# Optimization experiments

Hardware: AMD Instinct MI355X
Metric: run time of the kernel (lower is better)

The kernel has to match this reference:

```python
import jax, jax.numpy as jnp
import numpy as np

DIM = 2048
HEADS = 16
KV_HEADS = 4
DIM_HEAD = 128
INNER = HEADS * DIM_HEAD          # 2048
KV_INNER = KV_HEADS * DIM_HEAD    # 512
FF = 4 * DIM                      # 8192
QK_SCALE = 10.0                   # x-transformers default qk_norm_scale
B, S = 2, 2048


def layer_norm(x, g, b, eps=1e-5):
    m = jnp.mean(x, axis=-1, keepdims=True)
    v = jnp.mean((x - m) ** 2, axis=-1, keepdims=True)
    return (x - m) * jax.lax.rsqrt(v + eps) * g + b


def l2norm(t, eps=1e-12):
    n = jnp.sqrt(jnp.sum(t * t, axis=-1, keepdims=True))
    return t / jnp.maximum(n, eps)


def setup_inputs() -> dict:
    key = jax.random.key(0)
    ks = jax.random.split(key, 12)
    s = lambda fan_in: 1.0 / np.sqrt(fan_in)
    return {
        "x":     jax.random.normal(ks[0], (B, S, DIM), jnp.float32),
        "wq":    jax.random.normal(ks[1], (DIM, INNER), jnp.float32) * s(DIM),
        "wk":    jax.random.normal(ks[2], (DIM, KV_INNER), jnp.float32) * s(DIM),
        "wv":    jax.random.normal(ks[3], (DIM, KV_INNER), jnp.float32) * s(DIM),
        "wo":    jax.random.normal(ks[4], (INNER, DIM), jnp.float32) * s(INNER),
        "ln1_g": jnp.ones((DIM,), jnp.float32),
        "ln1_b": jnp.zeros((DIM,), jnp.float32),
        "w1":    jax.random.normal(ks[5], (DIM, FF), jnp.float32) * s(DIM),
        "b1":    jnp.zeros((FF,), jnp.float32),
        "lnf_g": jnp.ones((FF,), jnp.float32),
        "lnf_b": jnp.zeros((FF,), jnp.float32),
        "w2":    jax.random.normal(ks[6], (FF, DIM), jnp.float32) * s(FF),
        "b2":    jnp.zeros((DIM,), jnp.float32),
    }


def reference(x, wq, wk, wv, wo, ln1_g, ln1_b, w1, b1, lnf_g, lnf_b, w2, b2):
    b, s, _ = x.shape
    rep = HEADS // KV_HEADS
    # GQA projections
    q = (x @ wq).reshape(b, s, HEADS, DIM_HEAD).transpose(0, 2, 1, 3)      # [b,h,s,d]
    k = (x @ wk).reshape(b, s, KV_HEADS, DIM_HEAD).transpose(0, 2, 1, 3)   # [b,g,s,d]
    v = (x @ wv).reshape(b, s, KV_HEADS, DIM_HEAD).transpose(0, 2, 1, 3)
    # qk-norm: l2-normalize q/k along head dim, fixed scale
    q = l2norm(q)
    k = l2norm(k)
    k = jnp.repeat(k, rep, axis=1)  # expand kv heads to query heads
    v = jnp.repeat(v, rep, axis=1)
    scores = jnp.einsum("bhid,bhjd->bhij", q, k) * QK_SCALE
    attn = jax.nn.softmax(scores, axis=-1)
    o = jnp.einsum("bhij,bhjd->bhid", attn, v)
    o = o.transpose(0, 2, 1, 3).reshape(b, s, INNER) @ wo
    # post-attention LayerNorm (no residual in the source)
    h = layer_norm(o, ln1_g, ln1_b)
    # FFN: SiLU + post-activation LayerNorm (dropout inert in eval)
    f = jax.nn.silu(h @ w1 + b1)
    f = layer_norm(f, lnf_g, lnf_b)
    y = f @ w2 + b2
    # the source re-applies the SAME norm after the ffn
    return layer_norm(y, ln1_g, ln1_b)
```

## Files before the change

kernel.cpp:

```cpp
#include <hip/hip_runtime.h>


typedef __attribute__((ext_vector_type(8))) short short8;
typedef __attribute__((ext_vector_type(4))) float f32x4;
typedef __attribute__((ext_vector_type(16))) float f32x16;

__device__ __forceinline__ unsigned short f2bf(float f) {
  unsigned int u = __builtin_bit_cast(unsigned int, f);
  u += 0x7FFFu + ((u >> 16) & 1u);
  return (unsigned short)(u >> 16);
}
__device__ __forceinline__ float bf2f(unsigned short h) {
  unsigned int u = ((unsigned int)h) << 16;
  return __builtin_bit_cast(float, u);
}

typedef const void __attribute__((address_space(1)))* gas1_t;
typedef void __attribute__((address_space(3)))* las3_t;
#define GLDS16(g, l) \
  __builtin_amdgcn_global_load_lds((gas1_t)(const void*)(g), (las3_t)(void*)(l), 16, 0, 0)

__global__ __launch_bounds__(256) void cast_f32_bf16(const float* __restrict__ src,
                                                     unsigned short* __restrict__ dst,
                                                     int n) {
  int i = (blockIdx.x * 256 + threadIdx.x) * 4;
  if (i >= n) return;
  float4 f = *(const float4*)(src + i);
  uint2 u;
  u.x = (unsigned)f2bf(f.x) | ((unsigned)f2bf(f.y) << 16);
  u.y = (unsigned)f2bf(f.z) | ((unsigned)f2bf(f.w) << 16);
  *(uint2*)(dst + i) = u;
}

__global__ void transcast(const float* __restrict__ src, unsigned short* __restrict__ dst,
                          int R, int C, int dst_ld, int row_off) {
  __shared__ float t[32][33];
  const int tx = threadIdx.x, ty = threadIdx.y;
  const int c0 = blockIdx.x * 32, r0 = blockIdx.y * 32;
#pragma unroll
  for (int j = 0; j < 4; ++j)
    t[ty + j * 8][tx] = src[(size_t)(r0 + ty + j * 8) * C + c0 + tx];
  __syncthreads();
#pragma unroll
  for (int j = 0; j < 4; ++j)
    dst[(size_t)(row_off + c0 + ty + j * 8) * dst_ld + r0 + tx] = f2bf(t[tx][ty + j * 8]);
}

template <int KS>
__global__ __launch_bounds__(512, 1) void gemm8ph(const unsigned short* __restrict__ A,
                                                  const unsigned short* __restrict__ Bt,
                                                  unsigned short* __restrict__ C0,
                                                  unsigned short* __restrict__ C1,
                                                  int ldc, int Keff) {
  extern __shared__ char lds[];
  const int tid = threadIdx.x, l = tid & 63, w = tid >> 6;
  const int wr = w >> 2, wc = w & 3;
  const int gx = gridDim.x, gy = gridDim.y;
  const int did = blockIdx.y * gx + blockIdx.x;
  const int q = (gx * gy) >> 3;
  const int tcm = (did & 7) * q + (did >> 3);
  const int brow = (tcm % gy) * 256, bcol = (tcm / gy) * 256;
  const int ld = Keff * KS;
  const unsigned short* Aa = A + (size_t)brow * ld + blockIdx.z * Keff;
  const unsigned short* Bb = Bt + (size_t)bcol * ld + blockIdx.z * Keff;
  unsigned short* C = (KS == 1 || blockIdx.z == 0) ? C0 : C1;
  const int NT = Keff >> 6;

  const int slot = l >> 4;
  const int rowA = wr * 128 + (l & 15);
  const int aRd = ((((rowA << 2) | slot) << 4) ^ ((rowA & 7) << 4));
  const int rowB = wc * 64 + (l & 15);
  const int bRd = ((((rowB << 2) | slot) << 4) ^ ((rowB & 7) << 4));

  f32x4 acc[8][4];
#pragma unroll
  for (int m = 0; m < 8; ++m)
#pragma unroll
    for (int n = 0; n < 4; ++n) acc[m][n] = (f32x4){0.f, 0.f, 0.f, 0.f};

  auto stage = [&](int s) {
    const int tile = s >> 2, kind = s & 3;
    const int kofs = ((tile < NT) ? tile * 64 : 0) + (kind >> 1) * 32;
    const unsigned short* src = (kind & 1) ? Bb : Aa;
    char* dst = lds + (tile & 1) * 65536 + kind * 16384;
#pragma unroll
    for (int r = 0; r < 2; ++r) {
      const int g = r * 512 + tid;
      const int rw = ((g >> 3) << 1) | (((g >> 2) ^ (g >> 4)) & 1);
      const int sl = (g ^ rw) & 3;
      GLDS16(src + (size_t)rw * ld + kofs + sl * 8, dst + g * 16);
    }
  };

  stage(0); stage(1); stage(2); stage(3); stage(4); stage(5);
  asm volatile("s_waitcnt vmcnt(4)" ::: "memory");
  __builtin_amdgcn_s_barrier();

  for (int T = 0; T < NT; ++T) {
    char* cur = lds + (T & 1) * 65536;
#pragma unroll
    for (int ph = 0; ph < 4; ++ph) {
      const int ks = ph >> 1, mh = ph & 1;
      char* abase = cur + ks * 32768;
      char* bbase = cur + 16384 + ks * 32768;
      short8 af[4], bf[4];
#pragma unroll
      for (int n = 0; n < 4; ++n) bf[n] = *(const short8*)(bbase + bRd + n * 1024);
#pragma unroll
      for (int m = 0; m < 4; ++m) af[m] = *(const short8*)(abase + aRd + (mh * 4 + m) * 1024);
      stage(4 * T + ph + 6);
      __builtin_amdgcn_s_barrier();
      asm volatile("s_waitcnt lgkmcnt(0)" ::: "memory");
      __builtin_amdgcn_sched_barrier(0);
      __builtin_amdgcn_s_setprio(1);
#pragma unroll
      for (int m = 0; m < 4; ++m)
#pragma unroll
        for (int n = 0; n < 4; ++n)
          acc[mh * 4 + m][n] =
              __builtin_amdgcn_mfma_f32_16x16x32_bf16(af[m], bf[n], acc[mh * 4 + m][n], 0, 0, 0);
      __builtin_amdgcn_s_setprio(0);
      if (ph == 3) asm volatile("s_waitcnt vmcnt(4)" ::: "memory");
      __builtin_amdgcn_s_barrier();
    }
  }

#pragma unroll
  for (int m = 0; m < 8; ++m)
#pragma unroll
    for (int r = 0; r < 4; ++r) {
      const int row = brow + wr * 128 + m * 16 + (l >> 4) * 4 + r;
#pragma unroll
      for (int n = 0; n < 4; ++n) {
        const int col = bcol + wc * 64 + n * 16 + (l & 15);
        C[(size_t)row * ldc + col] = f2bf(acc[m][n][r]);
      }
    }
}

__global__ __launch_bounds__(256) void l2norm_qk(unsigned short* __restrict__ qkv) {
  const int wid = blockIdx.x * 4 + (threadIdx.x >> 6);
  const int l = threadIdx.x & 63;
  const int token = wid / 20, u = wid % 20;
  const int col = (u < 16) ? u * 128 : 2048 + (u - 16) * 128;
  unsigned short* p = qkv + (size_t)token * 3072 + col + l * 2;
  const float a = bf2f(p[0]), b = bf2f(p[1]);
  float ss = a * a + b * b;
#pragma unroll
  for (int m = 1; m < 64; m <<= 1) ss += __shfl_xor(ss, m);
  const float sc = ((u < 16) ? 10.f : 1.f) / fmaxf(sqrtf(ss), 1e-12f);
  p[0] = f2bf(a * sc);
  p[1] = f2bf(b * sc);
}

__global__ __launch_bounds__(256) void vtrans(const unsigned short* __restrict__ qkv,
                                              unsigned short* __restrict__ vt) {
  const int idx = blockIdx.x * 256 + threadIdx.x;
  const int s_ = idx & 2047;
  const int rest = idx >> 11;
  const int d = rest & 127;
  const int bg = rest >> 7;
  const int b = bg >> 2, g = bg & 3;
  vt[idx] = qkv[(size_t)(b * 2048 + s_) * 3072 + 2560 + g * 128 + d];
}

__global__ __launch_bounds__(512) void attn_kernel(const unsigned short* __restrict__ qkv,
                                                   const unsigned short* __restrict__ vt,
                                                   unsigned short* __restrict__ out) {
  extern __shared__ char smem[];
  const int tid = threadIdx.x, w = tid >> 6, l = tid & 63;
  const int hi = l >> 5, l31 = l & 31;

  const int n = blockIdx.x;
  const int np = (n & 7) * 32 + (n >> 3);
  const int qi = np & 7, bh = np >> 3;
  const int b = bh >> 4, h = bh & 15, g = h >> 2;
  const int q0 = qi * 256;

  const unsigned short* kbase = qkv + (size_t)(b * 2048) * 3072 + 2048 + g * 128;
  const unsigned short* vbase = vt + (size_t)(b * 4 + g) * 128 * 2048;

  short8 qf[8];
  {
    const unsigned short* qrow = qkv + (size_t)(b * 2048 + q0 + w * 32 + l31) * 3072 + h * 128;
#pragma unroll
    for (int st = 0; st < 8; ++st)
      qf[st] = *(const short8*)&qrow[st * 16 + hi * 8];
  }

  f32x16 o[4];
#pragma unroll
  for (int d0 = 0; d0 < 4; ++d0)
#pragma unroll
    for (int i = 0; i < 16; ++i) o[d0][i] = 0.f;
  float l_part = 0.f;

  const int krow = tid >> 3, kc = (tid & 7) * 2;
  const int vd = tid >> 2, vc = (tid & 3) * 2;
  const unsigned short* kg = kbase + (size_t)krow * 3072 + kc * 8;
  const unsigned short* vg = vbase + (size_t)vd * 2048 + vc * 8;
  const int ko0 = krow * 256 + ((kc ^ (krow & 15)) << 4);
  const int ko1 = krow * 256 + (((kc + 1) ^ (krow & 15)) << 4);
  const int vrp = vd >> 1, vcl = (vd & 1) * 8;
  const int vo0 = vrp * 256 + (((vcl + vc) ^ (vrp & 15)) << 4);
  const int vo1 = vrp * 256 + (((vcl + vc + 1) ^ (vrp & 15)) << 4);

  {
    uint4 k0 = *(const uint4*)kg, k1 = *(const uint4*)(kg + 8);
    uint4 v0 = *(const uint4*)vg, v1 = *(const uint4*)(vg + 8);
    char* Kb = smem;
    char* Vb = smem + 16384;
    *(uint4*)(Kb + ko0) = k0; *(uint4*)(Kb + ko1) = k1;
    *(uint4*)(Vb + vo0) = v0; *(uint4*)(Vb + vo1) = v1;
  }
  __syncthreads();

  const int swzk = l31 & 15;
  for (int t = 0; t < 32; ++t) {
    uint4 k0, k1, v0, v1;
    const bool more = (t + 1) < 32;
    if (more) {
      const size_t kvo = (size_t)(t + 1) * 64;
      k0 = *(const uint4*)(kg + kvo * 3072);
      k1 = *(const uint4*)(kg + kvo * 3072 + 8);
      v0 = *(const uint4*)(vg + kvo);
      v1 = *(const uint4*)(vg + kvo + 8);
    }

    char* Kb = smem + (t & 1) * 32768;
    char* Vb = Kb + 16384;

    f32x16 s0, s1;
#pragma unroll
    for (int i = 0; i < 16; ++i) { s0[i] = 0.f; s1[i] = 0.f; }
    __builtin_amdgcn_s_setprio(1);
#pragma unroll
    for (int st = 0; st < 8; ++st) {
      const int ch = st * 2 + hi;
      short8 kf0 = *(const short8*)(Kb + l31 * 256 + ((ch ^ swzk) << 4));
      short8 kf1 = *(const short8*)(Kb + (l31 + 32) * 256 + ((ch ^ swzk) << 4));
      s0 = __builtin_amdgcn_mfma_f32_32x32x16_bf16(kf0, qf[st], s0, 0, 0, 0);
      s1 = __builtin_amdgcn_mfma_f32_32x32x16_bf16(kf1, qf[st], s1, 0, 0, 0);
    }
    __builtin_amdgcn_s_setprio(0);

#pragma unroll
    for (int i = 0; i < 16; ++i) {
      s0[i] = __expf(s0[i] - 10.f);
      s1[i] = __expf(s1[i] - 10.f);
      l_part += s0[i] + s1[i];
    }

    short8 pa[4];
#pragma unroll
    for (int ks = 0; ks < 4; ++ks) {
      const f32x16& sv = (ks < 2) ? s0 : s1;
      const int base = (ks & 1) * 8;
      auto pk = [](float x, float y) -> unsigned {
        unsigned ux = __builtin_bit_cast(unsigned, x);
        unsigned uy = __builtin_bit_cast(unsigned, y);
        return ((uy + 0x8000u) & 0xFFFF0000u) | ((ux + 0x8000u) >> 16);
      };
      unsigned a = pk(sv[base + 0], sv[base + 1]);
      unsigned bq = pk(sv[base + 4], sv[base + 5]);
      unsigned c = pk(sv[base + 2], sv[base + 3]);
      unsigned d = pk(sv[base + 6], sv[base + 7]);
      unsigned as = __shfl_xor(a, 32), bs = __shfl_xor(bq, 32);
      unsigned cs = __shfl_xor(c, 32), ds = __shfl_xor(d, 32);
      uint4 wv;
      wv.x = (l < 32) ? a : bs;
      wv.y = (l < 32) ? c : ds;
      wv.z = (l < 32) ? as : bq;
      wv.w = (l < 32) ? cs : d;
      pa[ks] = __builtin_bit_cast(short8, wv);
    }

    __builtin_amdgcn_s_setprio(1);
#pragma unroll
    for (int ks = 0; ks < 4; ++ks) {
#pragma unroll
      for (int d0 = 0; d0 < 4; ++d0) {
        const int dd = d0 * 32 + l31;
        const int rp = dd >> 1;
        const int cl = ((dd & 1) * 8 + ks * 2 + hi) ^ (rp & 15);
        short8 vf = *(const short8*)(Vb + rp * 256 + (cl << 4));
        o[d0] = __builtin_amdgcn_mfma_f32_32x32x16_bf16(pa[ks], vf, o[d0], 0, 0, 0);
      }
    }
    __builtin_amdgcn_s_setprio(0);

    __syncthreads();
    if (more) {
      char* Kn = smem + ((t + 1) & 1) * 32768;
      char* Vn = Kn + 16384;
      *(uint4*)(Kn + ko0) = k0; *(uint4*)(Kn + ko1) = k1;
      *(uint4*)(Vn + vo0) = v0; *(uint4*)(Vn + vo1) = v1;
    }
    __syncthreads();
  }

  float ltot = l_part + __shfl_xor(l_part, 32);
  float linv = 1.f / ltot;
  const int tok_base = b * 2048 + q0 + w * 32;
#pragma unroll
  for (int r = 0; r < 16; ++r) {
    const int qr = (r & 3) + 8 * (r >> 2) + 4 * hi;
    const float li = __shfl(linv, qr);
    unsigned short* orow = out + (size_t)(tok_base + qr) * 2048 + h * 128 + l31;
#pragma unroll
    for (int d0 = 0; d0 < 4; ++d0)
      orow[d0 * 32] = f2bf(o[d0][r] * li);
  }
}

template <int NC, bool BIAS, bool SILU, bool OUTF32, bool SUM2>
__global__ __launch_bounds__(256) void ln_row(const unsigned short* __restrict__ src,
                                              const unsigned short* __restrict__ src2,
                                              unsigned short* __restrict__ dstb,
                                              float* __restrict__ dstf,
                                              const float* __restrict__ gamma,
                                              const float* __restrict__ beta,
                                              const float* __restrict__ bias) {
  constexpr int E = NC / 256;
  const int row = blockIdx.x, tid = threadIdx.x;
  const size_t base = (size_t)row * NC + tid * E;
  float v[E];
#pragma unroll
  for (int c = 0; c < E / 8; ++c) {
    uint4 u = *(const uint4*)(src + base + c * 8);
    const unsigned short* us = (const unsigned short*)&u;
#pragma unroll
    for (int j = 0; j < 8; ++j) v[c * 8 + j] = bf2f(us[j]);
  }
  if constexpr (SUM2) {
#pragma unroll
    for (int c = 0; c < E / 8; ++c) {
      uint4 u = *(const uint4*)(src2 + base + c * 8);
      const unsigned short* us = (const unsigned short*)&u;
#pragma unroll
      for (int j = 0; j < 8; ++j) v[c * 8 + j] += bf2f(us[j]);
    }
  }
  if constexpr (BIAS) {
#pragma unroll
    for (int i = 0; i < E; ++i) v[i] += bias[tid * E + i];
  }
  if constexpr (SILU) {
#pragma unroll
    for (int i = 0; i < E; ++i) v[i] = v[i] / (1.f + __expf(-v[i]));
  }
  float s = 0.f, q = 0.f;
#pragma unroll
  for (int i = 0; i < E; ++i) {
    s += v[i];
    q += v[i] * v[i];
  }
#pragma unroll
  for (int m = 1; m < 64; m <<= 1) {
    s += __shfl_xor(s, m);
    q += __shfl_xor(q, m);
  }
  __shared__ float rs[4], rq[4];
  if ((tid & 63) == 0) {
    rs[tid >> 6] = s;
    rq[tid >> 6] = q;
  }
  __syncthreads();
  s = rs[0] + rs[1] + rs[2] + rs[3];
  q = rq[0] + rq[1] + rq[2] + rq[3];
  const float mean = s / NC;
  const float rstd = rsqrtf(q / NC - mean * mean + 1e-5f);
#pragma unroll
  for (int i = 0; i < E; ++i)
    v[i] = (v[i] - mean) * rstd * gamma[tid * E + i] + beta[tid * E + i];
  if constexpr (OUTF32) {
#pragma unroll
    for (int c = 0; c < E / 4; ++c) {
      float4 f = {v[c * 4], v[c * 4 + 1], v[c * 4 + 2], v[c * 4 + 3]};
      *(float4*)(dstf + base + c * 4) = f;
    }
  } else {
#pragma unroll
    for (int c = 0; c < E / 8; ++c) {
      uint4 u;
      unsigned* up = (unsigned*)&u;
#pragma unroll
      for (int j = 0; j < 4; ++j)
        up[j] = (unsigned)f2bf(v[c * 8 + j * 2]) | ((unsigned)f2bf(v[c * 8 + j * 2 + 1]) << 16);
      *(uint4*)(dstb + base + c * 8) = u;
    }
  }
}

extern "C" void kernel_launch(void* const* d_in, const int* in_sizes, int n_in,
                              void* d_out, int out_size, void* d_ws, size_t ws_size,
                              hipStream_t stream) {
  (void)in_sizes; (void)n_in; (void)out_size; (void)ws_size;
  const float* x     = (const float*)d_in[0];
  const float* wq    = (const float*)d_in[1];
  const float* wk    = (const float*)d_in[2];
  const float* wv    = (const float*)d_in[3];
  const float* wo    = (const float*)d_in[4];
  const float* ln1_g = (const float*)d_in[5];
  const float* ln1_b = (const float*)d_in[6];
  const float* w1    = (const float*)d_in[7];
  const float* b1    = (const float*)d_in[8];
  const float* lnf_g = (const float*)d_in[9];
  const float* lnf_b = (const float*)d_in[10];
  const float* w2    = (const float*)d_in[11];
  const float* b2    = (const float*)d_in[12];

  unsigned short* ws = (unsigned short*)d_ws;
  unsigned short* wqkvT  = ws;
  unsigned short* woT    = wqkvT  + (size_t)3072 * 2048;
  unsigned short* w1T    = woT    + (size_t)2048 * 2048;
  unsigned short* w2T    = w1T    + (size_t)8192 * 2048;
  unsigned short* xb     = w2T    + (size_t)2048 * 8192;
  unsigned short* qkv    = xb     + (size_t)4096 * 2048;
  unsigned short* vt     = qkv    + (size_t)4096 * 3072;
  unsigned short* attn_o = vt     + (size_t)4096 * 512;
  unsigned short* f1     = attn_o + (size_t)4096 * 2048;

  (void)hipFuncSetAttribute((const void*)gemm8ph<1>,
                            hipFuncAttributeMaxDynamicSharedMemorySize, 131072);
  (void)hipFuncSetAttribute((const void*)gemm8ph<2>,
                            hipFuncAttributeMaxDynamicSharedMemorySize, 131072);
  (void)hipFuncSetAttribute((const void*)attn_kernel,
                            hipFuncAttributeMaxDynamicSharedMemorySize, 65536);

  const dim3 tb(32, 8);
  cast_f32_bf16<<<8192, 256, 0, stream>>>(x, xb, 4096 * 2048);
  transcast<<<dim3(64, 64),  tb, 0, stream>>>(wq, wqkvT, 2048, 2048, 2048, 0);
  transcast<<<dim3(16, 64),  tb, 0, stream>>>(wk, wqkvT, 2048, 512, 2048, 2048);
  transcast<<<dim3(16, 64),  tb, 0, stream>>>(wv, wqkvT, 2048, 512, 2048, 2560);
  transcast<<<dim3(64, 64),  tb, 0, stream>>>(wo, woT, 2048, 2048, 2048, 0);
  transcast<<<dim3(256, 64), tb, 0, stream>>>(w1, w1T, 2048, 8192, 2048, 0);
  transcast<<<dim3(64, 256), tb, 0, stream>>>(w2, w2T, 8192, 2048, 8192, 0);

  gemm8ph<1><<<dim3(12, 16, 1), 512, 131072, stream>>>(xb, wqkvT, qkv, nullptr, 3072, 2048);
  l2norm_qk<<<20480, 256, 0, stream>>>(qkv);
  vtrans<<<8192, 256, 0, stream>>>(qkv, vt);
  attn_kernel<<<256, 512, 65536, stream>>>(qkv, vt, attn_o);
  gemm8ph<2><<<dim3(8, 16, 2), 512, 131072, stream>>>(attn_o, woT, qkv, f1, 2048, 1024);
  ln_row<2048, false, false, false, true><<<4096, 256, 0, stream>>>(
      qkv, f1, xb, nullptr, ln1_g, ln1_b, nullptr);
  gemm8ph<1><<<dim3(32, 16, 1), 512, 131072, stream>>>(xb, w1T, f1, nullptr, 8192, 2048);
  ln_row<8192, true, true, false, false><<<4096, 256, 0, stream>>>(
      f1, nullptr, f1, nullptr, lnf_g, lnf_b, b1);
  gemm8ph<2><<<dim3(8, 16, 2), 512, 131072, stream>>>(f1, w2T, xb, attn_o, 2048, 4096);
  ln_row<2048, true, false, true, true><<<4096, 256, 0, stream>>>(
      xb, attn_o, nullptr, (float*)d_out, ln1_g, ln1_b, b2);
}
```

Measured before the change: 672.0 us.

## Software-pipeline LDS fragment reads ahead of MFMA phases in GEMM loop

Restructures the GEMM main loop so the LDS fragment loads for the next phase are issued before the current phase's 16 MFMAs. B fragments are also reused across the two M halves instead of being reloaded. The aim is to hide LDS read latency behind matrix math rather than stalling on lgkmcnt(0) before every MFMA batch. The cost is more live fragment registers, which may raise VGPR pressure, plus an extra barrier per phase.

```diff
diff --git a/kernel.cpp b/kernel.cpp
--- a/kernel.cpp
+++ b/kernel.cpp
@@ -92,38 +92,74 @@
     }
   };
 
+#define BAR() __builtin_amdgcn_s_barrier()
+#define LGKM0() do { asm volatile("s_waitcnt lgkmcnt(0)" ::: "memory"); \
+                     __builtin_amdgcn_sched_barrier(0); } while (0)
+#define SBAR() __builtin_amdgcn_sched_barrier(0)
+#define MFMA16(AF, BF, MO)                                                     \
+  do {                                                                         \
+    __builtin_amdgcn_s_setprio(1);                                             \
+    _Pragma("unroll") for (int m_ = 0; m_ < 4; ++m_)                           \
+        _Pragma("unroll") for (int n_ = 0; n_ < 4; ++n_)                       \
+            acc[(MO) + m_][n_] = __builtin_amdgcn_mfma_f32_16x16x32_bf16(      \
+                (AF)[m_], (BF)[n_], acc[(MO) + m_][n_], 0, 0, 0);              \
+    __builtin_amdgcn_s_setprio(0);                                             \
+  } while (0)
+
   stage(0); stage(1); stage(2); stage(3); stage(4); stage(5);
   asm volatile("s_waitcnt vmcnt(4)" ::: "memory");
-  __builtin_amdgcn_s_barrier();
+  BAR();
 
   for (int T = 0; T < NT; ++T) {
     char* cur = lds + (T & 1) * 65536;
-#pragma unroll
-    for (int ph = 0; ph < 4; ++ph) {
-      const int ks = ph >> 1, mh = ph & 1;
-      char* abase = cur + ks * 32768;
-      char* bbase = cur + 16384 + ks * 32768;
-      short8 af[4], bf[4];
-#pragma unroll
-      for (int n = 0; n < 4; ++n) bf[n] = *(const short8*)(bbase + bRd + n * 1024);
-#pragma unroll
-      for (int m = 0; m < 4; ++m) af[m] = *(const short8*)(abase + aRd + (mh * 4 + m) * 1024);
-      stage(4 * T + ph + 6);
-      __builtin_amdgcn_s_barrier();
-      asm volatile("s_waitcnt lgkmcnt(0)" ::: "memory");
-      __builtin_amdgcn_sched_barrier(0);
-      __builtin_amdgcn_s_setprio(1);
-#pragma unroll
-      for (int m = 0; m < 4; ++m)
-#pragma unroll
-        for (int n = 0; n < 4; ++n)
-          acc[mh * 4 + m][n] =
-              __builtin_amdgcn_mfma_f32_16x16x32_bf16(af[m], bf[n], acc[mh * 4 + m][n], 0, 0, 0);
-      __builtin_amdgcn_s_setprio(0);
-      if (ph == 3) asm volatile("s_waitcnt vmcnt(4)" ::: "memory");
-      __builtin_amdgcn_s_barrier();
-    }
-  }
+    char* A0 = cur, *B0 = cur + 16384, *A1 = cur + 32768, *B1 = cur + 49152;
+    short8 af0[4], af1[4], af2[4], af3[4], bf0[4], bf1[4];
+
+#pragma unroll
+    for (int n = 0; n < 4; ++n) bf0[n] = *(const short8*)(B0 + bRd + n * 1024);
+#pragma unroll
+    for (int m = 0; m < 4; ++m) af0[m] = *(const short8*)(A0 + aRd + m * 1024);
+    stage(4 * T + 6);
+    BAR();
+    LGKM0();
+#pragma unroll
+    for (int m = 0; m < 4; ++m) af1[m] = *(const short8*)(A0 + aRd + (4 + m) * 1024);
+    SBAR();
+    MFMA16(af0, bf0, 0);
+    BAR();
+
+    stage(4 * T + 7);
+    BAR();
+    LGKM0();
+#pragma unroll
+    for (int n = 0; n < 4; ++n) bf1[n] = *(const short8*)(B1 + bRd + n * 1024);
+#pragma unroll
+    for (int m = 0; m < 4; ++m) af2[m] = *(const short8*)(A1 + aRd + m * 1024);
+    SBAR();
+    MFMA16(af1, bf0, 4);
+    BAR();
+
+    stage(4 * T + 8);
+    BAR();
+    LGKM0();
+#pragma unroll
+    for (int m = 0; m < 4; ++m) af3[m] = *(const short8*)(A1 + aRd + (4 + m) * 1024);
+    SBAR();
+    MFMA16(af2, bf1, 0);
+    BAR();
+
+    stage(4 * T + 9);
+    BAR();
+    LGKM0();
+    SBAR();
+    MFMA16(af3, bf1, 4);
+    asm volatile("s_waitcnt vmcnt(4)" ::: "memory");
+    BAR();
+  }
+#undef BAR
+#undef LGKM0
+#undef SBAR
+#undef MFMA16
 
 #pragma unroll
   for (int m = 0; m < 8; ++m)
```

Result: faster. 645.2 us (-4.0%).
